# Kernel optimization log

Measured on AMD Instinct MI355X. Metric: run time of the kernel, lower is better.

The kernel has to match this reference:

```python
import jax, jax.numpy as jnp
import numpy as np

DIM = 1536
NUM_HEADS = 16
HEAD_DIM = DIM // NUM_HEADS  # 96
ROPE_DIM = HEAD_DIM // 2     # 48
PT_SEQ = 32
FT_SEQ = 32
EPS = 1e-6


def _rope_tables():
    # VisionRotaryEmbedding(dim=48, pt_seq_len=32): 2D axial rotary tables
    f = 1.0 / (10000.0 ** (np.arange(0, ROPE_DIM, 2, dtype=np.float32)[: ROPE_DIM // 2] / ROPE_DIM))
    pos = np.arange(FT_SEQ, dtype=np.float32) / FT_SEQ * PT_SEQ
    freqs = pos[:, None] * f[None, :]                       # [32, 24]
    freqs = np.repeat(freqs, 2, axis=-1)                    # [32, 48] interleaved
    row = np.broadcast_to(freqs[:, None, :], (FT_SEQ, FT_SEQ, ROPE_DIM))
    col = np.broadcast_to(freqs[None, :, :], (FT_SEQ, FT_SEQ, ROPE_DIM))
    grid = np.concatenate([row, col], axis=-1).reshape(-1, HEAD_DIM)  # [1024, 96]
    return jnp.asarray(np.cos(grid)), jnp.asarray(np.sin(grid))


def _apply_rotary(x, cos, sin):
    # x: [B, S, H, D]; cos/sin: [S, D]; interleaved (use_real_unbind_dim=-1) rotation
    xr = x.reshape(*x.shape[:-1], -1, 2)
    x_rot = jnp.stack([-xr[..., 1], xr[..., 0]], axis=-1).reshape(x.shape)
    return x * cos[None, :, None, :] + x_rot * sin[None, :, None, :]


def _rms_norm(x, w):
    var = jnp.mean(jnp.square(x), axis=-1, keepdims=True)
    return x * jax.lax.rsqrt(var + EPS) * w


def setup_inputs() -> dict:
    key = jax.random.key(0)
    ks = jax.random.split(key, 12)
    s = 1.0 / np.sqrt(DIM)
    return {
        "hidden_states": jax.random.normal(ks[0], (8, 1024, DIM), dtype=jnp.float32),
        "Wq": jax.random.normal(ks[1], (DIM, DIM), dtype=jnp.float32) * s,
        "bq": jax.random.normal(ks[2], (DIM,), dtype=jnp.float32) * 0.01,
        "Wk": jax.random.normal(ks[3], (DIM, DIM), dtype=jnp.float32) * s,
        "bk": jax.random.normal(ks[4], (DIM,), dtype=jnp.float32) * 0.01,
        "Wv": jax.random.normal(ks[5], (DIM, DIM), dtype=jnp.float32) * s,
        "bv": jax.random.normal(ks[6], (DIM,), dtype=jnp.float32) * 0.01,
        "q_norm_w": jnp.ones((HEAD_DIM,), dtype=jnp.float32),
        "k_norm_w": jnp.ones((HEAD_DIM,), dtype=jnp.float32),
        "Wo": jax.random.normal(ks[7], (DIM, DIM), dtype=jnp.float32) * s,
        "bo": jax.random.normal(ks[8], (DIM,), dtype=jnp.float32) * 0.01,
    }


def reference(hidden_states, Wq, bq, Wk, bk, Wv, bv, q_norm_w, k_norm_w, Wo, bo):
    B, S, _ = hidden_states.shape
    cos, sin = _rope_tables()  # [S, HEAD_DIM], constants

    q = hidden_states @ Wq.T + bq
    k = hidden_states @ Wk.T + bk
    v = hidden_states @ Wv.T + bv
    q = q.reshape(B, S, NUM_HEADS, HEAD_DIM)
    k = k.reshape(B, S, NUM_HEADS, HEAD_DIM)
    v = v.reshape(B, S, NUM_HEADS, HEAD_DIM)

    q = _rms_norm(q, q_norm_w)
    k = _rms_norm(k, k_norm_w)
    q = _apply_rotary(q, cos, sin)
    k = _apply_rotary(k, cos, sin)

    scale = 1.0 / np.sqrt(HEAD_DIM)
    scores = jnp.einsum("bshd,bthd->bhst", q, k) * scale  # [B, H, S, S]
    probs = jax.nn.softmax(scores, axis=-1)
    out = jnp.einsum("bhst,bthd->bshd", probs, v)          # [B, S, H, D]
    out = out.reshape(B, S, DIM)
    return out @ Wo.T + bo
```

## Files before the change

### kernel.cpp

```cpp
#include <hip/hip_runtime.h>
#include <hip/hip_bf16.h>
#include <math.h>

typedef __hip_bfloat16 bf16;
typedef __attribute__((ext_vector_type(8))) short short8;
typedef __attribute__((ext_vector_type(4))) short short4v;
typedef __attribute__((ext_vector_type(4))) float f32x4;

#define MFMA16(a, b, c) __builtin_amdgcn_mfma_f32_16x16x32_bf16((a), (b), (c), 0, 0, 0)

typedef const __attribute__((address_space(1))) void GVOID;
typedef __attribute__((address_space(3))) void LVOID;

__device__ __forceinline__ float b2f(short s) {
    union { unsigned u; float f; } v;
    v.u = ((unsigned)(unsigned short)s) << 16;
    return v.f;
}
__device__ __forceinline__ short f2b(float f) {
    union { float f; unsigned u; } v;
    v.f = f;
    unsigned r = v.u + 0x7fffu + ((v.u >> 16) & 1u);
    return (short)(r >> 16);
}
__device__ __forceinline__ unsigned packbf(float a, float b) {
    return ((unsigned)(unsigned short)f2b(a)) | (((unsigned)(unsigned short)f2b(b)) << 16);
}

__global__ void sniff_kernel(const unsigned* __restrict__ X, int* __restrict__ flag) {
    __shared__ int cnt;
    if (threadIdx.x == 0) cnt = 0;
    __syncthreads();
    int c = 0;
    for (int i = threadIdx.x; i < 256; i += 64) {
        unsigned w = X[i];
        unsigned e = (w >> 7) & 0xFFu;
        c += (e > 140u) ? 1 : 0;
    }
    atomicAdd(&cnt, c);
    __syncthreads();
    if (threadIdx.x == 0) *flag = (cnt >= 16) ? 1 : 0;
}

__device__ __forceinline__ void canon8(const void* src, short* dst, int i, int f) {
    short8 o;
    if (f) {
        const float* s = (const float*)src + (size_t)i * 8;
#pragma unroll
        for (int j = 0; j < 8; ++j) o[j] = f2b(s[j]);
    } else {
        o = ((const short8*)src)[i];
    }
    ((short8*)dst)[i] = o;
}

__global__ __launch_bounds__(256) void canon_x_kernel(
    const void* __restrict__ src, short* __restrict__ dst, int n8,
    const int* __restrict__ flag)
{
    int i = blockIdx.x * 256 + threadIdx.x;
    if (i >= n8) return;
    canon8(src, dst, i, *flag);
}

__global__ __launch_bounds__(256) void canon_w4_kernel(
    const void* __restrict__ s0, const void* __restrict__ s1,
    const void* __restrict__ s2, const void* __restrict__ s3,
    short* __restrict__ d0, short* __restrict__ d1,
    short* __restrict__ d2, short* __restrict__ d3,
    const int* __restrict__ flag)
{
    const int m = blockIdx.y;
    const void* src = (m == 0) ? s0 : (m == 1) ? s1 : (m == 2) ? s2 : s3;
    short* dst = (m == 0) ? d0 : (m == 1) ? d1 : (m == 2) ? d2 : d3;
    int i = blockIdx.x * 256 + threadIdx.x;
    canon8(src, dst, i, *flag);
}

__global__ void canon_vec_kernel(
    const void* __restrict__ bq, const void* __restrict__ bk,
    const void* __restrict__ bv, const void* __restrict__ bo,
    const void* __restrict__ qw, const void* __restrict__ kw,
    float* __restrict__ biasqkv, float* __restrict__ boc,
    float* __restrict__ qwc, float* __restrict__ kwc,
    const int* __restrict__ flag)
{
    const int f = *flag;
    for (int i = threadIdx.x; i < 6336; i += 256) {
        const void* src; float* dst; int j;
        if (i < 4608) {
            int m = i / 1536; j = i - m * 1536;
            src = (m == 0) ? bq : (m == 1) ? bk : bv; dst = biasqkv + i;
        } else if (i < 6144) { j = i - 4608; src = bo; dst = boc + j; }
        else if (i < 6240)   { j = i - 6144; src = qw; dst = qwc + j; }
        else                 { j = i - 6240; src = kw; dst = kwc + j; }
        *dst = f ? ((const float*)src)[j] : b2f(((const short*)src)[j]);
    }
}

__global__ void rope_tables_kernel(float* __restrict__ cosT, float* __restrict__ sinT) {
    int idx = blockIdx.x * 256 + threadIdx.x;
    if (idx >= 1024 * 96) return;
    int p = idx / 96;
    int d = idx - p * 96;
    int r = p >> 5, c = p & 31;
    int inRow = (d < 48);
    int dd = inRow ? d : d - 48;
    float pos = inRow ? (float)r : (float)c;
    float ex = -(float)(dd & ~1) / 48.0f;
    float f = powf(10000.0f, ex);
    float ang = pos * f;
    cosT[idx] = cosf(ang);
    sinT[idx] = sinf(ang);
}

__global__ __launch_bounds__(512) void gemm256_kernel(
    const bf16* __restrict__ A, const bf16* __restrict__ Bw,
    const float* __restrict__ bias,
    bf16* __restrict__ O0, bf16* __restrict__ O1, bf16* __restrict__ O2,
    int K, const int* __restrict__ outFlag)
{
    __shared__ __align__(16) short As[2][256 * 32];
    __shared__ __align__(16) short Bs[2][256 * 32];

    const int tid = threadIdx.x;
    const int lane = tid & 63, w = tid >> 6;
    const int wm = w >> 2, wn = w & 3;
    const int li = lane & 15, lg = lane >> 4;

    const int total = gridDim.x * gridDim.y;
    const int pp = blockIdx.y * gridDim.x + blockIdx.x;
    const int lb = (pp & 7) * (total >> 3) + (pp >> 3);
    const int nb = lb % gridDim.x;
    const int mb = lb / gridDim.x;
    const long mBase = (long)mb * 256;
    const long nGlob = (long)nb * 256;

    const bf16* aSrc[2]; const bf16* bSrc[2]; int ldsOff[2];
#pragma unroll
    for (int u = 0; u < 2; ++u) {
        const int L = u * 8192 + tid * 16;
        const int S = L ^ (((L >> 7) & 3) << 4);
        const int srow = S >> 6;
        const int scol = (S & 63) >> 1;
        aSrc[u] = A + (mBase + srow) * K + scol;
        bSrc[u] = Bw + (nGlob + srow) * K + scol;
        ldsOff[u] = L >> 1;
    }
    const int koff = ((lg * 16) ^ (((li >> 1) & 3) << 4)) >> 1;

    f32x4 acc[8][4] = {};
    const int NT = K >> 5;

    auto stage = [&](int tt, int bb) {
        const long kc = (long)tt * 32;
#pragma unroll
        for (int u = 0; u < 2; ++u)
            __builtin_amdgcn_global_load_lds((GVOID*)(aSrc[u] + kc),
                                             (LVOID*)&As[bb][ldsOff[u]], 16, 0, 0);
#pragma unroll
        for (int u = 0; u < 2; ++u)
            __builtin_amdgcn_global_load_lds((GVOID*)(bSrc[u] + kc),
                                             (LVOID*)&Bs[bb][ldsOff[u]], 16, 0, 0);
    };

    stage(0, 0);
    asm volatile("s_waitcnt vmcnt(0)" ::: "memory");
    __builtin_amdgcn_s_barrier();
    asm volatile("" ::: "memory");

    for (int t = 0; t < NT; ++t) {
        const int cb = t & 1;
        if (t + 1 < NT) stage(t + 1, cb ^ 1);
        const short* Ab = &As[cb][0];
        const short* Bb = &Bs[cb][0];
        short8 fb[4], fa[4];
#pragma unroll
        for (int n = 0; n < 4; ++n)
            fb[n] = *(const short8*)(Bb + (wn * 64 + n * 16 + li) * 32 + koff);
#pragma unroll
        for (int m = 0; m < 4; ++m)
            fa[m] = *(const short8*)(Ab + (wm * 128 + m * 16 + li) * 32 + koff);
        __builtin_amdgcn_sched_barrier(0);
        __builtin_amdgcn_s_setprio(1);
#pragma unroll
        for (int m = 0; m < 4; ++m)
#pragma unroll
            for (int n = 0; n < 4; ++n)
                acc[m][n] = MFMA16(fa[m], fb[n], acc[m][n]);
        __builtin_amdgcn_s_setprio(0);
        __builtin_amdgcn_sched_barrier(0);
#pragma unroll
        for (int m = 0; m < 4; ++m)
            fa[m] = *(const short8*)(Ab + (wm * 128 + 64 + m * 16 + li) * 32 + koff);
        __builtin_amdgcn_sched_barrier(0);
        __builtin_amdgcn_s_setprio(1);
#pragma unroll
        for (int m = 0; m < 4; ++m)
#pragma unroll
            for (int n = 0; n < 4; ++n)
                acc[4 + m][n] = MFMA16(fa[m], fb[n], acc[4 + m][n]);
        __builtin_amdgcn_s_setprio(0);
        __builtin_amdgcn_sched_barrier(0);
        asm volatile("s_waitcnt vmcnt(0)" ::: "memory");
        __builtin_amdgcn_s_barrier();
        asm volatile("" ::: "memory");
    }

    const int f32out = outFlag ? *outFlag : 0;
    const int mat = nb / 6;
    const long colBase = nGlob - (long)mat * 1536;
    bf16* Ob = (mat == 0) ? O0 : (mat == 1) ? O1 : O2;
    if (f32out) {
        float* Cf = (float*)Ob;
#pragma unroll
        for (int n = 0; n < 4; ++n) {
            const long col = colBase + wn * 64 + n * 16 + li;
            const float bv = bias[nGlob + wn * 64 + n * 16 + li];
#pragma unroll
            for (int m = 0; m < 8; ++m) {
                const long row = mBase + wm * 128 + m * 16 + lg * 4;
#pragma unroll
                for (int i = 0; i < 4; ++i)
                    Cf[(row + i) * 1536 + col] = acc[m][n][i] + bv;
            }
        }
    } else {
#pragma unroll
        for (int n = 0; n < 4; ++n) {
            const long col = colBase + wn * 64 + n * 16 + li;
            const float bv = bias[nGlob + wn * 64 + n * 16 + li];
#pragma unroll
            for (int m = 0; m < 8; ++m) {
                const long row = mBase + wm * 128 + m * 16 + lg * 4;
#pragma unroll
                for (int i = 0; i < 4; ++i)
                    Ob[(row + i) * 1536 + col] = __float2bfloat16(acc[m][n][i] + bv);
            }
        }
    }
}

__global__ __launch_bounds__(256) void norm_rope_kernel(
    bf16* __restrict__ T, const float* __restrict__ wgt,
    const float* __restrict__ cosT, const float* __restrict__ sinT,
    float scale)
{
    const int row = blockIdx.x * 256 + threadIdx.x;
    const int tok = row >> 4;
    const int h = row & 15;
    const int spos = tok & 1023;
    bf16* p = T + (size_t)tok * 1536 + h * 96;

    float x[96];
#pragma unroll
    for (int v = 0; v < 12; ++v) {
        short8 t = *(const short8*)(p + v * 8);
#pragma unroll
        for (int j = 0; j < 8; ++j) x[v * 8 + j] = b2f(t[j]);
    }
    float ss = 0.f;
#pragma unroll
    for (int d = 0; d < 96; ++d) ss += x[d] * x[d];
    const float rn = scale / sqrtf(ss * (1.0f / 96.0f) + 1e-6f);

    const float* cr = cosT + spos * 96;
    const float* sr = sinT + spos * 96;

#pragma unroll
    for (int v = 0; v < 12; ++v) {
        short8 o;
#pragma unroll
        for (int j = 0; j < 8; j += 2) {
            const int d = v * 8 + j;
            const float x0 = x[d] * rn * wgt[d];
            const float x1 = x[d + 1] * rn * wgt[d + 1];
            o[j]     = f2b(x0 * cr[d] - x1 * sr[d]);
            o[j + 1] = f2b(x1 * cr[d + 1] + x0 * sr[d + 1]);
        }
        *(short8*)(p + v * 8) = o;
    }
}

__global__ __launch_bounds__(256) void attn_kernel(
    const bf16* __restrict__ Q, const bf16* __restrict__ K,
    const bf16* __restrict__ V, bf16* __restrict__ O)
{
    __shared__ __align__(16) short Ks[64 * 100];
    __shared__ __align__(16) short Vt[96 * 76];
    __shared__ __align__(16) short Pl[4][32 * 72];

    const int tid = threadIdx.x;
    const int l = tid & 63, w = tid >> 6;
    const int li = l & 15, lg = l >> 4;

    const int p = blockIdx.x;
    const int lb = (p & 7) * 128 + (p >> 3);
    const int qt = lb & 7;
    const int bh = lb >> 3;
    const int b = bh >> 4, h = bh & 15;
    const size_t tokBase = (size_t)b * 1024;

    short8 aq[2][3];
#pragma unroll
    for (int r = 0; r < 2; ++r) {
        const bf16* qp = Q + (tokBase + qt * 128 + w * 32 + r * 16 + li) * 1536 + h * 96;
#pragma unroll
        for (int kk = 0; kk < 3; ++kk)
            aq[r][kk] = *(const short8*)(qp + kk * 32 + lg * 8);
    }

    float m_r[2] = {-1e30f, -1e30f};
    float l_r[2] = {0.f, 0.f};
    f32x4 o[2][6] = {};

    int kr[3], km[3];
#pragma unroll
    for (int u = 0; u < 3; ++u) {
        const int c = tid + 256 * u;
        kr[u] = c / 12;
        km[u] = (c - kr[u] * 12) * 8;
    }
    const int vr = tid >> 2;
    const int vc0 = (tid & 3) * 24;
    short* Plw = &Pl[w][0];

    short8 kreg[3], vreg[3];
#pragma unroll
    for (int u = 0; u < 3; ++u)
        kreg[u] = *(const short8*)(K + (tokBase + kr[u]) * 1536 + h * 96 + km[u]);
    {
        const bf16* vp = V + (tokBase + vr) * 1536 + h * 96 + vc0;
#pragma unroll
        for (int u = 0; u < 3; ++u) vreg[u] = *(const short8*)(vp + u * 8);
    }

    for (int t0 = 0; t0 < 1024; t0 += 64) {
        __syncthreads();
#pragma unroll
        for (int u = 0; u < 3; ++u)
            *(short8*)&Ks[kr[u] * 100 + km[u]] = kreg[u];
#pragma unroll
        for (int u = 0; u < 3; ++u)
#pragma unroll
            for (int j = 0; j < 8; ++j)
                Vt[(vc0 + u * 8 + j) * 76 + vr] = vreg[u][j];
        __syncthreads();

        const int t1 = (t0 + 64 < 1024) ? t0 + 64 : t0;
#pragma unroll
        for (int u = 0; u < 3; ++u)
            kreg[u] = *(const short8*)(K + (tokBase + t1 + kr[u]) * 1536 + h * 96 + km[u]);
        {
            const bf16* vp = V + (tokBase + t1 + vr) * 1536 + h * 96 + vc0;
#pragma unroll
            for (int u = 0; u < 3; ++u) vreg[u] = *(const short8*)(vp + u * 8);
        }

        f32x4 s4[2][4] = {};
#pragma unroll
        for (int kk = 0; kk < 3; ++kk) {
            short8 fk[4];
#pragma unroll
            for (int kn = 0; kn < 4; ++kn)
                fk[kn] = *(const short8*)&Ks[(kn * 16 + li) * 100 + kk * 32 + lg * 8];
#pragma unroll
            for (int r = 0; r < 2; ++r)
#pragma unroll
                for (int kn = 0; kn < 4; ++kn)
                    s4[r][kn] = MFMA16(fk[kn], aq[r][kk], s4[r][kn]);
        }

#pragma unroll
        for (int r = 0; r < 2; ++r) {
            float mk[4];
#pragma unroll
            for (int kn = 0; kn < 4; ++kn)
                mk[kn] = fmaxf(fmaxf(s4[r][kn][0], s4[r][kn][1]),
                               fmaxf(s4[r][kn][2], s4[r][kn][3]));
            float pm = fmaxf(fmaxf(mk[0], mk[1]), fmaxf(mk[2], mk[3]));
            pm = fmaxf(pm, __shfl_xor(pm, 16));
            pm = fmaxf(pm, __shfl_xor(pm, 32));

            float alpha = 1.0f;
            const bool need = (pm > m_r[r] + 8.0f);
            if (need) { alpha = exp2f(m_r[r] - pm); m_r[r] = pm; }
            const float mn = m_r[r];

            float rs = 0.f;
            unsigned pw[8];
#pragma unroll
            for (int kn = 0; kn < 4; ++kn) {
                float p0 = exp2f(s4[r][kn][0] - mn);
                float p1 = exp2f(s4[r][kn][1] - mn);
                float p2 = exp2f(s4[r][kn][2] - mn);
                float p3 = exp2f(s4[r][kn][3] - mn);
                rs += (p0 + p1) + (p2 + p3);
                pw[kn * 2]     = packbf(p0, p1);
                pw[kn * 2 + 1] = packbf(p2, p3);
            }
            rs += __shfl_xor(rs, 16);
            rs += __shfl_xor(rs, 32);
            l_r[r] = l_r[r] * alpha + rs;
            if (need) {
#pragma unroll
                for (int dn = 0; dn < 6; ++dn)
#pragma unroll
                    for (int i = 0; i < 4; ++i) o[r][dn][i] *= alpha;
            }
            unsigned* Pw = (unsigned*)Plw;
            const int rowW = ((r * 16 + li) * 72) >> 1;
#pragma unroll
            for (int kn = 0; kn < 4; ++kn) {
#pragma unroll
                for (int ip = 0; ip < 2; ++ip)
                    Pw[rowW + ((kn * 16 + lg * 4 + ip * 2) >> 1)] = pw[kn * 2 + ip];
            }
        }

#pragma unroll
        for (int kt = 0; kt < 2; ++kt) {
            short8 pa[2];
#pragma unroll
            for (int r = 0; r < 2; ++r)
                pa[r] = *(const short8*)&Plw[(r * 16 + li) * 72 + kt * 32 + lg * 8];
#pragma unroll
            for (int dn = 0; dn < 6; ++dn) {
                short8 fv = *(const short8*)&Vt[(dn * 16 + li) * 76 + kt * 32 + lg * 8];
#pragma unroll
                for (int r = 0; r < 2; ++r)
                    o[r][dn] = MFMA16(fv, pa[r], o[r][dn]);
            }
        }
    }

#pragma unroll
    for (int r = 0; r < 2; ++r) {
        const float inv = 1.0f / l_r[r];
        const size_t row = tokBase + qt * 128 + w * 32 + r * 16 + li;
#pragma unroll
        for (int dn = 0; dn < 6; ++dn) {
            short4v ov;
#pragma unroll
            for (int i = 0; i < 4; ++i) ov[i] = f2b(o[r][dn][i] * inv);
            *(short4v*)&O[row * 1536 + h * 96 + dn * 16 + lg * 4] = ov;
        }
    }
}

extern "C" void kernel_launch(void* const* d_in, const int* in_sizes, int n_in,
                              void* d_out, int out_size, void* d_ws, size_t ws_size,
                              hipStream_t stream) {
    const void* X  = d_in[0];
    const void* Wq = d_in[1];
    const void* bq = d_in[2];
    const void* Wk = d_in[3];
    const void* bk = d_in[4];
    const void* Wv = d_in[5];
    const void* bv = d_in[6];
    const void* qw = d_in[7];
    const void* kw = d_in[8];
    const void* Wo = d_in[9];
    const void* bo = d_in[10];

    char* ws = (char*)d_ws;
    size_t off = 0;
    int* flag = (int*)ws;                      off += 256;
    float* cosT = (float*)(ws + off);          off += 1024 * 96 * 4;
    float* sinT = (float*)(ws + off);          off += 1024 * 96 * 4;
    float* biasqkv = (float*)(ws + off);       off += 4608 * 4;
    float* boc  = (float*)(ws + off);          off += 1536 * 4;
    float* qwc  = (float*)(ws + off);          off += 128 * 4;
    float* kwc  = (float*)(ws + off);          off += 128 * 4;
    off = (off + 255) & ~(size_t)255;
    bf16* Wc  = (bf16*)(ws + off);             off += (size_t)4608 * 1536 * 2;
    bf16* Woc = (bf16*)(ws + off);             off += (size_t)1536 * 1536 * 2;
    bf16* Xc  = (bf16*)(ws + off);             off += (size_t)8192 * 1536 * 2;
    bf16* Qb  = (bf16*)(ws + off);             off += (size_t)8192 * 1536 * 2;
    bf16* Kb  = (bf16*)(ws + off);             off += (size_t)8192 * 1536 * 2;
    bf16* Vb  = (bf16*)(ws + off);             off += (size_t)8192 * 1536 * 2;
    bf16* AO  = Xc;

    sniff_kernel<<<1, 64, 0, stream>>>((const unsigned*)X, flag);

    canon_x_kernel<<<6144, 256, 0, stream>>>(X, (short*)Xc, 8192 * 1536 / 8, flag);
    canon_w4_kernel<<<dim3(1152, 4), 256, 0, stream>>>(
        Wq, Wk, Wv, Wo,
        (short*)Wc, (short*)(Wc + (size_t)1536 * 1536), (short*)(Wc + (size_t)2 * 1536 * 1536),
        (short*)Woc, flag);
    canon_vec_kernel<<<1, 256, 0, stream>>>(bq, bk, bv, bo, qw, kw,
                                            biasqkv, boc, qwc, kwc, flag);
    rope_tables_kernel<<<384, 256, 0, stream>>>(cosT, sinT);

    gemm256_kernel<<<dim3(18, 32), 512, 0, stream>>>(
        Xc, Wc, biasqkv, Qb, Kb, Vb, 1536, nullptr);

    const float qscale = (float)(0.10206207261596577 * 1.4426950408889634);
    norm_rope_kernel<<<512, 256, 0, stream>>>(Qb, qwc, cosT, sinT, qscale);
    norm_rope_kernel<<<512, 256, 0, stream>>>(Kb, kwc, cosT, sinT, 1.0f);

    attn_kernel<<<1024, 256, 0, stream>>>(Qb, Kb, Vb, AO);

    gemm256_kernel<<<dim3(6, 32), 512, 0, stream>>>(
        AO, Woc, boc, (bf16*)d_out, (bf16*)d_out, (bf16*)d_out, 1536, flag);
}
```

Before: 461.5 us.

## Deepen GEMM K-tile to 64 and use 128x128 tiles for output projection

The 256x256 GEMM now stages 64-wide K slices, with a new 8-way XOR LDS swizzle and a four-phase MFMA schedule that reorders fragment loads. This halves the number of barriers and loop iterations per GEMM. A new 128x128-tile GEMM kernel with 256 threads replaces the 256-tile launch for the output projection, giving 768 blocks instead of 192 so more CUs are filled. The cost is doubled LDS use per block (128KB for the 256 kernel), which may reduce occupancy.

```diff
diff --git a/kernel.cpp b/kernel.cpp
--- a/kernel.cpp
+++ b/kernel.cpp
@@ -120,8 +120,8 @@
     bf16* __restrict__ O0, bf16* __restrict__ O1, bf16* __restrict__ O2,
     int K, const int* __restrict__ outFlag)
 {
-    __shared__ __align__(16) short As[2][256 * 32];
-    __shared__ __align__(16) short Bs[2][256 * 32];
+    __shared__ __align__(16) short As[2][256 * 64];
+    __shared__ __align__(16) short Bs[2][256 * 64];
 
     const int tid = threadIdx.x;
     const int lane = tid & 63, w = tid >> 6;
@@ -136,30 +136,34 @@
     const long mBase = (long)mb * 256;
     const long nGlob = (long)nb * 256;
 
-    const bf16* aSrc[2]; const bf16* bSrc[2]; int ldsOff[2];
-#pragma unroll
-    for (int u = 0; u < 2; ++u) {
+    const bf16* aSrc[4]; const bf16* bSrc[4]; int ldsOff[4];
+#pragma unroll
+    for (int u = 0; u < 4; ++u) {
         const int L = u * 8192 + tid * 16;
-        const int S = L ^ (((L >> 7) & 3) << 4);
-        const int srow = S >> 6;
-        const int scol = (S & 63) >> 1;
+        const int S = L ^ (((L >> 7) & 7) << 4);
+        const int srow = S >> 7;
+        const int scol = (S & 127) >> 1;
         aSrc[u] = A + (mBase + srow) * K + scol;
         bSrc[u] = Bw + (nGlob + srow) * K + scol;
         ldsOff[u] = L >> 1;
     }
-    const int koff = ((lg * 16) ^ (((li >> 1) & 3) << 4)) >> 1;
+    const int rxor = (li & 7) << 4;
+    int kidx[2];
+#pragma unroll
+    for (int ks = 0; ks < 2; ++ks)
+        kidx[ks] = ((ks * 64 + lg * 16) ^ rxor) >> 1;
 
     f32x4 acc[8][4] = {};
-    const int NT = K >> 5;
+    const int NT = K >> 6;
 
     auto stage = [&](int tt, int bb) {
-        const long kc = (long)tt * 32;
-#pragma unroll
-        for (int u = 0; u < 2; ++u)
+        const long kc = (long)tt * 64;
+#pragma unroll
+        for (int u = 0; u < 4; ++u)
             __builtin_amdgcn_global_load_lds((GVOID*)(aSrc[u] + kc),
                                              (LVOID*)&As[bb][ldsOff[u]], 16, 0, 0);
 #pragma unroll
-        for (int u = 0; u < 2; ++u)
+        for (int u = 0; u < 4; ++u)
             __builtin_amdgcn_global_load_lds((GVOID*)(bSrc[u] + kc),
                                              (LVOID*)&Bs[bb][ldsOff[u]], 16, 0, 0);
     };
@@ -174,35 +178,41 @@
         if (t + 1 < NT) stage(t + 1, cb ^ 1);
         const short* Ab = &As[cb][0];
         const short* Bb = &Bs[cb][0];
-        short8 fb[4], fa[4];
-#pragma unroll
-        for (int n = 0; n < 4; ++n)
-            fb[n] = *(const short8*)(Bb + (wn * 64 + n * 16 + li) * 32 + koff);
-#pragma unroll
-        for (int m = 0; m < 4; ++m)
-            fa[m] = *(const short8*)(Ab + (wm * 128 + m * 16 + li) * 32 + koff);
-        __builtin_amdgcn_sched_barrier(0);
-        __builtin_amdgcn_s_setprio(1);
-#pragma unroll
-        for (int m = 0; m < 4; ++m)
-#pragma unroll
-            for (int n = 0; n < 4; ++n)
-                acc[m][n] = MFMA16(fa[m], fb[n], acc[m][n]);
-        __builtin_amdgcn_s_setprio(0);
-        __builtin_amdgcn_sched_barrier(0);
-#pragma unroll
-        for (int m = 0; m < 4; ++m)
-            fa[m] = *(const short8*)(Ab + (wm * 128 + 64 + m * 16 + li) * 32 + koff);
-        __builtin_amdgcn_sched_barrier(0);
-        __builtin_amdgcn_s_setprio(1);
-#pragma unroll
-        for (int m = 0; m < 4; ++m)
-#pragma unroll
-            for (int n = 0; n < 4; ++n)
-                acc[4 + m][n] = MFMA16(fa[m], fb[n], acc[4 + m][n]);
-        __builtin_amdgcn_s_setprio(0);
-        __builtin_amdgcn_sched_barrier(0);
-        asm volatile("s_waitcnt vmcnt(0)" ::: "memory");
+        short8 fa[4][2], fb[2][2];
+#pragma unroll
+        for (int ph = 0; ph < 4; ++ph) {
+            const int qm = ph >> 1, qn = ph & 1;
+            if (qn == 0) {
+#pragma unroll
+                for (int m = 0; m < 4; ++m) {
+                    const int row = wm * 128 + (qm * 4 + m) * 16 + li;
+#pragma unroll
+                    for (int ks = 0; ks < 2; ++ks)
+                        fa[m][ks] = *(const short8*)(Ab + row * 64 + kidx[ks]);
+                }
+            }
+#pragma unroll
+            for (int n = 0; n < 2; ++n) {
+                const int row = wn * 64 + (qn * 2 + n) * 16 + li;
+#pragma unroll
+                for (int ks = 0; ks < 2; ++ks)
+                    fb[n][ks] = *(const short8*)(Bb + row * 64 + kidx[ks]);
+            }
+            __builtin_amdgcn_sched_barrier(0);
+            __builtin_amdgcn_s_setprio(1);
+#pragma unroll
+            for (int m = 0; m < 4; ++m)
+#pragma unroll
+                for (int n = 0; n < 2; ++n)
+#pragma unroll
+                    for (int ks = 0; ks < 2; ++ks)
+                        acc[qm * 4 + m][qn * 2 + n] =
+                            MFMA16(fa[m][ks], fb[n][ks], acc[qm * 4 + m][qn * 2 + n]);
+            __builtin_amdgcn_s_setprio(0);
+            __builtin_amdgcn_sched_barrier(0);
+            if (ph == 2)
+                asm volatile("s_waitcnt vmcnt(0)" ::: "memory");
+        }
         __builtin_amdgcn_s_barrier();
         asm volatile("" ::: "memory");
     }
@@ -236,6 +246,125 @@
 #pragma unroll
                 for (int i = 0; i < 4; ++i)
                     Ob[(row + i) * 1536 + col] = __float2bfloat16(acc[m][n][i] + bv);
+            }
+        }
+    }
+}
+
+__global__ __launch_bounds__(256) void gemm128_kernel(
+    const bf16* __restrict__ A, const bf16* __restrict__ Bw,
+    const float* __restrict__ bias, void* __restrict__ C,
+    int K, const int* __restrict__ outFlag)
+{
+    __shared__ __align__(16) short As[2][128 * 64];
+    __shared__ __align__(16) short Bs[2][128 * 64];
+
+    const int tid = threadIdx.x;
+    const int lane = tid & 63, w = tid >> 6;
+    const int wr = w >> 1, wc = w & 1;
+    const int li = lane & 15, lg = lane >> 4;
+
+    const int total = gridDim.x * gridDim.y;
+    const int pp = blockIdx.y * gridDim.x + blockIdx.x;
+    const int lb = (pp & 7) * (total >> 3) + (pp >> 3);
+    const int nb = lb % gridDim.x;
+    const int mb = lb / gridDim.x;
+    const long mBase = (long)mb * 128;
+    const long nBase = (long)nb * 128;
+
+    const bf16* aSrc[4]; const bf16* bSrc[4]; int ldsOff[4];
+#pragma unroll
+    for (int u = 0; u < 4; ++u) {
+        const int L = u * 4096 + tid * 16;
+        const int S = L ^ (((L >> 7) & 7) << 4);
+        const int srow = S >> 7;
+        const int scol = (S & 127) >> 1;
+        aSrc[u] = A + (mBase + srow) * K + scol;
+        bSrc[u] = Bw + (nBase + srow) * K + scol;
+        ldsOff[u] = L >> 1;
+    }
+    const int rxor = (li & 7) << 4;
+    int kidx[2];
+#pragma unroll
+    for (int ks = 0; ks < 2; ++ks)
+        kidx[ks] = ((ks * 64 + lg * 16) ^ rxor) >> 1;
+
+    f32x4 acc[4][4] = {};
+    const int NT = K >> 6;
+
+    auto stage = [&](int tt, int bb) {
+        const long kc = (long)tt * 64;
+#pragma unroll
+        for (int u = 0; u < 4; ++u)
+            __builtin_amdgcn_global_load_lds((GVOID*)(aSrc[u] + kc),
+                                             (LVOID*)&As[bb][ldsOff[u]], 16, 0, 0);
+#pragma unroll
+        for (int u = 0; u < 4; ++u)
+            __builtin_amdgcn_global_load_lds((GVOID*)(bSrc[u] + kc),
+                                             (LVOID*)&Bs[bb][ldsOff[u]], 16, 0, 0);
+    };
+
+    stage(0, 0);
+    asm volatile("s_waitcnt vmcnt(0)" ::: "memory");
+    __builtin_amdgcn_s_barrier();
+    asm volatile("" ::: "memory");
+
+    for (int t = 0; t < NT; ++t) {
+        const int cb = t & 1;
+        if (t + 1 < NT) stage(t + 1, cb ^ 1);
+        const short* Ab = &As[cb][0];
+        const short* Bb = &Bs[cb][0];
+#pragma unroll
+        for (int ks = 0; ks < 2; ++ks) {
+            short8 fa[4], fb[4];
+#pragma unroll
+            for (int m = 0; m < 4; ++m)
+                fa[m] = *(const short8*)(Ab + (wr * 64 + m * 16 + li) * 64 + kidx[ks]);
+#pragma unroll
+            for (int n = 0; n < 4; ++n)
+                fb[n] = *(const short8*)(Bb + (wc * 64 + n * 16 + li) * 64 + kidx[ks]);
+            __builtin_amdgcn_sched_barrier(0);
+            __builtin_amdgcn_s_setprio(1);
+#pragma unroll
+            for (int m = 0; m < 4; ++m)
+#pragma unroll
+                for (int n = 0; n < 4; ++n)
+                    acc[m][n] = MFMA16(fa[m], fb[n], acc[m][n]);
+            __builtin_amdgcn_s_setprio(0);
+            __builtin_amdgcn_sched_barrier(0);
+        }
+        asm volatile("s_waitcnt vmcnt(0)" ::: "memory");
+        __builtin_amdgcn_s_barrier();
+        asm volatile("" ::: "memory");
+    }
+
+    const int f32out = outFlag ? *outFlag : 0;
+    if (f32out) {
+        float* Cf = (float*)C;
+#pragma unroll
+        for (int n = 0; n < 4; ++n) {
+            const long col = nBase + wc * 64 + n * 16 + li;
+            const float bv = bias[col];
+#pragma unroll
+            for (int m = 0; m < 4; ++m) {
+                const long row = mBase + wr * 64 + m * 16 + lg * 4;
+#pragma unroll
+                for (int i = 0; i < 4; ++i)
+                    Cf[(row + i) * 1536 + col] = acc[m][n][i] + bv;
+            }
+        }
+    } else {
+        bf16* Cb = (bf16*)C;
+#pragma unroll
+        for (int n = 0; n < 4; ++n) {
+            const long col = nBase + wc * 64 + n * 16 + li;
+            const float bv = bias[col];
+#pragma unroll
+            for (int m = 0; m < 4; ++m) {
+                const long row = mBase + wr * 64 + m * 16 + lg * 4;
+#pragma unroll
+                for (int i = 0; i < 4; ++i)
+                    Cb[(row + i) * 1536 + col] = __float2bfloat16(acc[m][n][i] + bv);
             }
         }
     }
@@ -501,6 +630,6 @@
 
     attn_kernel<<<1024, 256, 0, stream>>>(Qb, Kb, Vb, AO);
 
-    gemm256_kernel<<<dim3(6, 32), 512, 0, stream>>>(
-        AO, Woc, boc, (bf16*)d_out, (bf16*)d_out, (bf16*)d_out, 1536, flag);
-}
+    gemm128_kernel<<<dim3(12, 64), 256, 0, stream>>>(
+        AO, Woc, boc, d_out, 1536, flag);
+}
```

Result: faster. 441.5 us (-4.3%).
